# Kernel tuning notes

Hardware: AMD Instinct MI355X
Metric: run time of the kernel (lower is better)

The kernel has to match this reference:

```python
import jax, jax.numpy as jnp
import numpy as np

NUM_EMB = 8192
DIM = 64
DECAY = 0.99
EPS = 1e-05
COMMIT = 0.25


def setup_inputs() -> dict:
    key = jax.random.key(0)
    k1, k2, k3 = jax.random.split(key, 3)
    inputs = jax.random.normal(k1, (8, 4096, DIM), jnp.float32)
    weight = jax.random.normal(k2, (NUM_EMB, DIM), jnp.float32)
    ema_cluster_count = jnp.ones((NUM_EMB,), jnp.float32)
    ema_weight_sum = jax.random.normal(k3, (NUM_EMB, DIM), jnp.float32)
    return {
        'inputs': inputs,
        'weight': weight,
        'ema_cluster_count': ema_cluster_count,
        'ema_weight_sum': ema_weight_sum,
    }


def reference(inputs, weight, ema_cluster_count, ema_weight_sum):
    flat = inputs.reshape(-1, DIM)  # [N, D]
    distances = (
        jnp.sum(flat ** 2, axis=1, keepdims=True)
        + jnp.sum(weight ** 2, axis=1)
        - 2.0 * flat @ weight.T
    )
    idx = jnp.argmin(distances, axis=1)  # [N] int

    # EMA stats (training branch): one-hot column sums == segment counts,
    # encodings.T @ flat == segment sums of inputs by code index.
    counts = jax.ops.segment_sum(
        jnp.ones(flat.shape[0], jnp.float32), idx, num_segments=NUM_EMB)
    new_cc = ema_cluster_count * DECAY + (1.0 - DECAY) * counts
    emb_sum = jax.ops.segment_sum(flat, idx, num_segments=NUM_EMB)
    new_ws = ema_weight_sum * DECAY + (1.0 - DECAY) * emb_sum

    n = jnp.sum(new_cc)
    smoothed = (new_cc + EPS) / (n + NUM_EMB * EPS) * n
    new_weight = new_ws / smoothed[:, None]  # updated codebook [K, D]

    quantized_raw = new_weight[idx].reshape(inputs.shape)
    e_latent_loss = jnp.mean((jax.lax.stop_gradient(quantized_raw) - inputs) ** 2)
    vq_loss = COMMIT * e_latent_loss

    avg_probs = counts / flat.shape[0]
    perplexity = jnp.exp(-jnp.sum(avg_probs * jnp.log(avg_probs + 1e-10)))

    # straight-through estimator
    quantized = inputs + jax.lax.stop_gradient(quantized_raw - inputs)
    return quantized, vq_loss, idx, perplexity, new_weight, new_cc, new_ws
```

## Files before the change

### kernel.cpp

```cpp
#include <hip/hip_runtime.h>
#include <math.h>

typedef _Float16 f16x8 __attribute__((ext_vector_type(8)));
typedef float f32x4 __attribute__((ext_vector_type(4)));

#define NROWS 32768
#define KEMB  8192

#define DECAYF 0.99f
#define OMDF   0.01f

#define OUT_Q    0
#define OUT_LOSS 2097152
#define OUT_IDX  2097153
#define OUT_PERP 2129921
#define OUT_NW   2129922
#define OUT_NCC  2654210
#define OUT_NWS  2662402

#define WS_N      0
#define WS_ENT    1
#define WS_COUNTS 4
#define WS_EMB    8196
#define WS_IDX    532484
#define WS_W2H    565252
#define WS_WFRAG  573444
#define WS_ZERO_UNITS 532484

__device__ __forceinline__ float sq_rn(float v) { return __fmul_rn(v, v); }

__device__ __forceinline__ float npsumsq64(const float* vbuf) {
  float a[8];
#pragma unroll
  for (int j = 0; j < 8; ++j) a[j] = sq_rn(vbuf[j]);
#pragma unroll
  for (int m = 1; m < 8; ++m)
#pragma unroll
    for (int j = 0; j < 8; ++j) a[j] = __fadd_rn(a[j], sq_rn(vbuf[m*8 + j]));
  return __fadd_rn(__fadd_rn(__fadd_rn(a[0],a[1]), __fadd_rn(a[2],a[3])),
                   __fadd_rn(__fadd_rn(a[4],a[5]), __fadd_rn(a[6],a[7])));
}

__device__ __forceinline__ void split_f16(float x, _Float16& hi, _Float16& lo) {
  hi = (_Float16)x;
  float r = __fsub_rn(x, (float)hi);
  lo = (_Float16)r;
}

__global__ __launch_bounds__(256) void prep_kernel(const float* __restrict__ wg,
                                                   float* __restrict__ ws) {
  const int tid = blockIdx.x * 256 + threadIdx.x;
  if (tid < KEMB) {
    const float* src = wg + (size_t)tid * 64;
    float vbuf[64];
#pragma unroll
    for (int f = 0; f < 16; ++f) {
      float4 v = *(const float4*)(src + f*4);
      vbuf[f*4+0]=v.x; vbuf[f*4+1]=v.y; vbuf[f*4+2]=v.z; vbuf[f*4+3]=v.w;
    }
    ws[WS_W2H + tid] = __fmul_rn(0.5f, npsumsq64(vbuf));
  } else if (tid < KEMB + 65536) {
    const int u = tid - KEMB;
    const int K = u >> 3, g = u & 7;
    const int n = K & 15, P = K >> 4;
    const int slot = (g&3)*16 + n, shi = g >> 2;
    const float* src = wg + (size_t)K*64 + g*8;
    float4 v0 = *(const float4*)src, v1 = *(const float4*)(src + 4);
    float vv[8] = {v0.x,v0.y,v0.z,v0.w,v1.x,v1.y,v1.z,v1.w};
    f16x8 hi, lo;
#pragma unroll
    for (int j = 0; j < 8; ++j) { _Float16 h, l; split_f16(vv[j], h, l); hi[j]=h; lo[j]=l; }
    _Float16* wf = (_Float16*)(ws + WS_WFRAG);
    *(f16x8*)&wf[((size_t)(P*4 + shi)*64 + slot)*8]     = hi;
    *(f16x8*)&wf[((size_t)(P*4 + 2 + shi)*64 + slot)*8] = lo;
  }
}

#define COMPUTE_PANEL(I, B0, B1, B2, B3, W2)                                        \
  {                                                                                 \
    const f32x4 cin = {(W2), (W2), (W2), (W2)};                                     \
    f32x4 acc[4];                                                                   \
    _Pragma("unroll")                                                               \
    for (int rt = 0; rt < 4; ++rt) acc[rt] = __builtin_amdgcn_mfma_f32_16x16x32_f16(a[rt][0], (B0), cin, 0,0,0); \
    _Pragma("unroll")                                                               \
    for (int rt = 0; rt < 4; ++rt) acc[rt] = __builtin_amdgcn_mfma_f32_16x16x32_f16(a[rt][1], (B1), acc[rt], 0,0,0); \
    _Pragma("unroll")                                                               \
    for (int rt = 0; rt < 4; ++rt) acc[rt] = __builtin_amdgcn_mfma_f32_16x16x32_f16(a[rt][2], (B0), acc[rt], 0,0,0); \
    _Pragma("unroll")                                                               \
    for (int rt = 0; rt < 4; ++rt) acc[rt] = __builtin_amdgcn_mfma_f32_16x16x32_f16(a[rt][3], (B1), acc[rt], 0,0,0); \
    _Pragma("unroll")                                                               \
    for (int rt = 0; rt < 4; ++rt) acc[rt] = __builtin_amdgcn_mfma_f32_16x16x32_f16(a[rt][0], (B2), acc[rt], 0,0,0); \
    _Pragma("unroll")                                                               \
    for (int rt = 0; rt < 4; ++rt) acc[rt] = __builtin_amdgcn_mfma_f32_16x16x32_f16(a[rt][1], (B3), acc[rt], 0,0,0); \
    const int kk = (I)*64 + cg*16 + n16;                                            \
    _Pragma("unroll")                                                               \
    for (int rt = 0; rt < 4; ++rt)                                                  \
      _Pragma("unroll")                                                             \
      for (int reg = 0; reg < 4; ++reg) {                                           \
        const float dist = acc[rt][reg];                                            \
        const int bi = rt*4 + reg;                                                  \
        if (dist < best[bi]) { best[bi] = dist; bestk[bi] = kk; }                   \
      }                                                                             \
  }

#define LOADB(I, C0, C1, C2, C3, CW)                                                \
  {                                                                                 \
    const size_t base = ((size_t)((I)*4 + cg) * 256) * 8 + lane8;                   \
    C0 = *(const f16x8*)&wfrag[base];                                               \
    C1 = *(const f16x8*)&wfrag[base + 512];                                         \
    C2 = *(const f16x8*)&wfrag[base + 1024];                                        \
    C3 = *(const f16x8*)&wfrag[base + 1536];                                        \
    CW = w2hg[(I)*64 + cg*16 + n16];                                                \
  }

__global__ __launch_bounds__(512) void argmin_kernel(const float* __restrict__ xg,
                                                     float* __restrict__ out,
                                                     float* __restrict__ ws) {
  __shared__ __align__(16) _Float16 xp[8*4*64*8];
  __shared__ float md[128*4];
  __shared__ int   mk[128*4];
  __shared__ int   bkL[128];

  const int t    = threadIdx.x;
  const int lane = t & 63, wv = t >> 6;
  const int quad = lane >> 4, n16 = lane & 15;
  const int rg = wv >> 2, cg = wv & 3;
  const int row0 = blockIdx.x * 128;
  const _Float16* __restrict__ wfrag = (const _Float16*)(ws + WS_WFRAG);
  const float* __restrict__ w2hg = ws + WS_W2H;

#pragma unroll
  for (int it = 0; it < 2; ++it) {
    const int u  = t + 512*it;
    const int rp = u >> 7, n = (u >> 3) & 15, g = u & 7;
    const float* src = xg + (size_t)(row0 + rp*16 + n)*64 + g*8;
    float4 v0 = *(const float4*)src, v1 = *(const float4*)(src + 4);
    float vv[8] = {v0.x,v0.y,v0.z,v0.w,v1.x,v1.y,v1.z,v1.w};
    f16x8 hi, lo;
#pragma unroll
    for (int j = 0; j < 8; ++j) { _Float16 h, l; split_f16(-vv[j], h, l); hi[j]=h; lo[j]=l; }
    const int slot = (g&3)*16 + n, shi = g >> 2;
    *(f16x8*)&xp[(((rp*4) + shi)*64 + slot)*8]     = hi;
    *(f16x8*)&xp[(((rp*4) + 2 + shi)*64 + slot)*8] = lo;
  }
  __syncthreads();

  f16x8 a[4][4];
#pragma unroll
  for (int rt = 0; rt < 4; ++rt)
#pragma unroll
    for (int s = 0; s < 4; ++s)
      a[rt][s] = *(const f16x8*)&xp[(((rg*4+rt)*4 + s)*64 + lane)*8];

  float best[16]; int bestk[16];
#pragma unroll
  for (int i = 0; i < 16; ++i) { best[i] = INFINITY; bestk[i] = 0; }

  const size_t lane8 = (size_t)lane * 8;
  f16x8 p0, p1, p2, p3, q0, q1, q2, q3;
  float pw, qw;
  LOADB(0, p0, p1, p2, p3, pw);

  for (int it = 0; it < 128; it += 2) {
    LOADB(it+1, q0, q1, q2, q3, qw);
    COMPUTE_PANEL(it, p0, p1, p2, p3, pw);
    if (it + 2 < 128) LOADB(it+2, p0, p1, p2, p3, pw);
    COMPUTE_PANEL(it+1, q0, q1, q2, q3, qw);
  }

#pragma unroll
  for (int bi = 0; bi < 16; ++bi) {
    float bd = best[bi]; int bk = bestk[bi];
#pragma unroll
    for (int m = 1; m < 16; m <<= 1) {
      const float od = __shfl_xor(bd, m, 64);
      const int   ok = __shfl_xor(bk, m, 64);
      if (od < bd || (od == bd && ok < bk)) { bd = od; bk = ok; }
    }
    best[bi] = bd; bestk[bi] = bk;
  }
  if (n16 == 0) {
#pragma unroll
    for (int rt = 0; rt < 4; ++rt)
#pragma unroll
      for (int reg = 0; reg < 4; ++reg) {
        const int row = rg*64 + rt*16 + quad*4 + reg;
        md[row*4 + cg] = best[rt*4+reg];
        mk[row*4 + cg] = bestk[rt*4+reg];
      }
  }
  __syncthreads();

  if (t < 128) {
    const int row = t;
    float bd = md[row*4]; int bk = mk[row*4];
#pragma unroll
    for (int u = 1; u < 4; ++u) {
      const float d2 = md[row*4 + u]; const int k2 = mk[row*4 + u];
      if (d2 < bd || (d2 == bd && k2 < bk)) { bd = d2; bk = k2; }
    }
    out[OUT_IDX + row0 + row] = (float)bk;
    ((int*)ws)[WS_IDX + row0 + row] = bk;
    bkL[row] = bk;
    atomicAdd(&ws[WS_COUNTS + bk], 1.0f);
  }
  __syncthreads();

#pragma unroll 4
  for (int r = 0; r < 16; ++r) {
    const int row = wv*16 + r;
    const int k = bkL[row];
    atomicAdd(&ws[WS_EMB + (size_t)k*64 + lane],
              xg[(size_t)(row0 + row)*64 + lane]);
  }
}

__global__ __launch_bounds__(256) void stats_kernel(const float* __restrict__ cc,
                                                    float* __restrict__ out,
                                                    float* __restrict__ ws) {
  const int t = threadIdx.x;
  float v1 = 0.0f, v2 = 0.0f;
#pragma unroll
  for (int i = 0; i < 32; ++i) {
    const int k = i*256 + t;
    const float cnt = ws[WS_COUNTS + k];
    const float ncc = __fadd_rn(__fmul_rn(DECAYF, cc[k]), __fmul_rn(OMDF, cnt));
    out[OUT_NCC + k] = ncc;
    const float p = cnt * (1.0f/32768.0f);
    v1 += ncc;
    v2 += __fmul_rn(p, logf(__fadd_rn(p, 1e-10f)));
  }
#pragma unroll
  for (int off = 32; off > 0; off >>= 1) {
    v1 += __shfl_down(v1, off);
    v2 += __shfl_down(v2, off);
  }
  __shared__ float s1[4], s2[4];
  const int lane = t & 63, wid = t >> 6;
  if (lane == 0) { s1[wid] = v1; s2[wid] = v2; }
  __syncthreads();
  if (t == 0) {
    ws[WS_N]   = (s1[0]+s1[1]) + (s1[2]+s1[3]);
    ws[WS_ENT] = (s2[0]+s2[1]) + (s2[2]+s2[3]);
  }
}

__global__ __launch_bounds__(256) void update_kernel(const float* __restrict__ ws0,
                                                     float* __restrict__ out,
                                                     float* __restrict__ ws) {
  const int e4 = blockIdx.x * 256 + threadIdx.x;
  const int k = e4 >> 4;
  const float n = ws[WS_N];
  const float ncc = out[OUT_NCC + k];
  const float smoothed = __fmul_rn(__fadd_rn(ncc, 1e-5f) / __fadd_rn(n, 0.08192f), n);
  const float inv_s = 1.0f / smoothed;
  float4 w0 = *(const float4*)(ws0 + (size_t)e4*4);
  float4 em = *(const float4*)(ws + WS_EMB + (size_t)e4*4);
  float wv[4] = {w0.x, w0.y, w0.z, w0.w};
  float ev[4] = {em.x, em.y, em.z, em.w};
  float nwsv[4], nwv[4];
#pragma unroll
  for (int i = 0; i < 4; ++i) {
    nwsv[i] = __fadd_rn(__fmul_rn(DECAYF, wv[i]), __fmul_rn(OMDF, ev[i]));
    nwv[i]  = nwsv[i] / smoothed;
  }
  (void)inv_s;
  float4 onws = {nwsv[0], nwsv[1], nwsv[2], nwsv[3]};
  float4 onw  = {nwv[0],  nwv[1],  nwv[2],  nwv[3]};
  *(float4*)(out + OUT_NWS + (size_t)e4*4) = onws;
  *(float4*)(out + OUT_NW  + (size_t)e4*4) = onw;
  if (e4 == 0) out[OUT_PERP] = expf(-ws[WS_ENT]);
}

__global__ __launch_bounds__(256) void quant_kernel(const float* __restrict__ xg,
                                                    float* __restrict__ out,
                                                    float* __restrict__ ws) {
  const int t = threadIdx.x;
  const int* idxb = (const int*)ws + WS_IDX;
  float v = 0.0f;
#pragma unroll
  for (int j = 0; j < 4; ++j) {
    const int e4 = (j*512 + blockIdx.x)*256 + t;
    const int row = e4 >> 4, d = (e4 & 15) * 4;
    const int k = idxb[row];
    const float* nw = out + OUT_NW + (size_t)k*64 + d;
    float2 q0 = *(const float2*)nw, q1 = *(const float2*)(nw + 2);
    float4 x = *(const float4*)(xg + (size_t)e4*4);
    float qv[4] = {q0.x, q0.y, q1.x, q1.y};
    float xv[4] = {x.x, x.y, x.z, x.w};
    float4 o;
    float ov[4];
#pragma unroll
    for (int i = 0; i < 4; ++i) {
      const float df = __fsub_rn(qv[i], xv[i]);
      ov[i] = __fadd_rn(xv[i], df);
      v = fmaf(df, df, v);
    }
    o.x = ov[0]; o.y = ov[1]; o.z = ov[2]; o.w = ov[3];
    *(float4*)(out + OUT_Q + (size_t)e4*4) = o;
  }
#pragma unroll
  for (int off = 32; off > 0; off >>= 1) v += __shfl_down(v, off);
  __shared__ float sm[4];
  const int lane = t & 63, wid = t >> 6;
  if (lane == 0) sm[wid] = v;
  __syncthreads();
  if (t == 0) ws[WS_COUNTS + blockIdx.x] = (sm[0]+sm[1]) + (sm[2]+sm[3]);
}

__global__ void final_kernel(float* __restrict__ out, const float* __restrict__ ws) {
  const int t = threadIdx.x;
  float v = 0.0f;
#pragma unroll
  for (int i = 0; i < 8; ++i) v += ws[WS_COUNTS + i*64 + t];
#pragma unroll
  for (int off = 32; off > 0; off >>= 1) v += __shfl_down(v, off);
  if (t == 0) out[OUT_LOSS] = __fmul_rn(0.25f, v / 2097152.0f);
}

extern "C" void kernel_launch(void* const* d_in, const int* in_sizes, int n_in,
                              void* d_out, int out_size, void* d_ws, size_t ws_size,
                              hipStream_t stream) {
  (void)in_sizes; (void)n_in; (void)out_size; (void)ws_size;
  const float* x   = (const float*)d_in[0];
  const float* w   = (const float*)d_in[1];
  const float* cc  = (const float*)d_in[2];
  const float* ws0 = (const float*)d_in[3];
  float* out = (float*)d_out;
  float* ws  = (float*)d_ws;

  hipMemsetAsync(d_ws, 0, (size_t)WS_ZERO_UNITS * 4, stream);
  hipLaunchKernelGGL(prep_kernel,   dim3(288),  dim3(256), 0, stream, w, ws);
  hipLaunchKernelGGL(argmin_kernel, dim3(256),  dim3(512), 0, stream, x, out, ws);
  hipLaunchKernelGGL(stats_kernel,  dim3(1),    dim3(256), 0, stream, cc, out, ws);
  hipLaunchKernelGGL(update_kernel, dim3(512),  dim3(256), 0, stream, ws0, out, ws);
  hipLaunchKernelGGL(quant_kernel,  dim3(512),  dim3(256), 0, stream, x, out, ws);
  hipLaunchKernelGGL(final_kernel,  dim3(1),    dim3(64),  0, stream, out, ws);
}
```

Measured before the change: 187.8 us.

## Remove memset and stats kernel by folding zeroing, total-count algebra, and entropy into neighbors

Workspace zeroing moves from a separate memset into a grid-stride loop inside prep_kernel. The single-block stats kernel is removed. The total n is computed in prep as 0.99*sum(cc) plus 0.01*N, since the counts always sum to the row count. New cluster counts are computed inside update_kernel, and the entropy and perplexity reduction moves into final_kernel. This cuts two launches and a serial single-block step from the critical path. The loss partials now reuse the W2H workspace region, which is safe only because W2H is dead after argmin.

```diff
diff --git a/kernel.cpp b/kernel.cpp
--- a/kernel.cpp
+++ b/kernel.cpp
@@ -26,6 +26,7 @@
 #define WS_W2H    565252
 #define WS_WFRAG  573444
 #define WS_ZERO_UNITS 532484
+#define WS_LOSSP  (WS_W2H + 1024)
 
 __device__ __forceinline__ float sq_rn(float v) { return __fmul_rn(v, v); }
 
@@ -48,8 +49,10 @@
 }
 
 __global__ __launch_bounds__(256) void prep_kernel(const float* __restrict__ wg,
+                                                   const float* __restrict__ cc,
                                                    float* __restrict__ ws) {
   const int tid = blockIdx.x * 256 + threadIdx.x;
+  for (int i = tid; i < WS_ZERO_UNITS; i += 73728) ws[i] = 0.0f;
   if (tid < KEMB) {
     const float* src = wg + (size_t)tid * 64;
     float vbuf[64];
@@ -74,6 +77,18 @@
     *(f16x8*)&wf[((size_t)(P*4 + shi)*64 + slot)*8]     = hi;
     *(f16x8*)&wf[((size_t)(P*4 + 2 + shi)*64 + slot)*8] = lo;
   }
+  if (blockIdx.x == 0) {
+    float s = 0.0f;
+    for (int i = threadIdx.x; i < KEMB; i += 256) s += cc[i];
+#pragma unroll
+    for (int off = 32; off > 0; off >>= 1) s += __shfl_down(s, off);
+    __shared__ float sw[4];
+    const int lane = threadIdx.x & 63, wid = threadIdx.x >> 6;
+    if (lane == 0) sw[wid] = s;
+    __syncthreads();
+    if (threadIdx.x == 0)
+      ws[WS_N] = __fadd_rn(__fmul_rn(DECAYF, (sw[0]+sw[1])+(sw[2]+sw[3])), 327.68f);
+  }
 }
 
 #define COMPUTE_PANEL(I, B0, B1, B2, B3, W2)                                        \
@@ -215,45 +230,17 @@
   }
 }
 
-__global__ __launch_bounds__(256) void stats_kernel(const float* __restrict__ cc,
-                                                    float* __restrict__ out,
-                                                    float* __restrict__ ws) {
-  const int t = threadIdx.x;
-  float v1 = 0.0f, v2 = 0.0f;
-#pragma unroll
-  for (int i = 0; i < 32; ++i) {
-    const int k = i*256 + t;
-    const float cnt = ws[WS_COUNTS + k];
-    const float ncc = __fadd_rn(__fmul_rn(DECAYF, cc[k]), __fmul_rn(OMDF, cnt));
-    out[OUT_NCC + k] = ncc;
-    const float p = cnt * (1.0f/32768.0f);
-    v1 += ncc;
-    v2 += __fmul_rn(p, logf(__fadd_rn(p, 1e-10f)));
-  }
-#pragma unroll
-  for (int off = 32; off > 0; off >>= 1) {
-    v1 += __shfl_down(v1, off);
-    v2 += __shfl_down(v2, off);
-  }
-  __shared__ float s1[4], s2[4];
-  const int lane = t & 63, wid = t >> 6;
-  if (lane == 0) { s1[wid] = v1; s2[wid] = v2; }
-  __syncthreads();
-  if (t == 0) {
-    ws[WS_N]   = (s1[0]+s1[1]) + (s1[2]+s1[3]);
-    ws[WS_ENT] = (s2[0]+s2[1]) + (s2[2]+s2[3]);
-  }
-}
-
 __global__ __launch_bounds__(256) void update_kernel(const float* __restrict__ ws0,
+                                                     const float* __restrict__ cc,
                                                      float* __restrict__ out,
                                                      float* __restrict__ ws) {
   const int e4 = blockIdx.x * 256 + threadIdx.x;
   const int k = e4 >> 4;
   const float n = ws[WS_N];
-  const float ncc = out[OUT_NCC + k];
+  const float cnt = ws[WS_COUNTS + k];
+  const float ncc = __fadd_rn(__fmul_rn(DECAYF, cc[k]), __fmul_rn(OMDF, cnt));
+  if ((e4 & 15) == 0) out[OUT_NCC + k] = ncc;
   const float smoothed = __fmul_rn(__fadd_rn(ncc, 1e-5f) / __fadd_rn(n, 0.08192f), n);
-  const float inv_s = 1.0f / smoothed;
   float4 w0 = *(const float4*)(ws0 + (size_t)e4*4);
   float4 em = *(const float4*)(ws + WS_EMB + (size_t)e4*4);
   float wv[4] = {w0.x, w0.y, w0.z, w0.w};
@@ -264,12 +251,10 @@
     nwsv[i] = __fadd_rn(__fmul_rn(DECAYF, wv[i]), __fmul_rn(OMDF, ev[i]));
     nwv[i]  = nwsv[i] / smoothed;
   }
-  (void)inv_s;
   float4 onws = {nwsv[0], nwsv[1], nwsv[2], nwsv[3]};
   float4 onw  = {nwv[0],  nwv[1],  nwv[2],  nwv[3]};
   *(float4*)(out + OUT_NWS + (size_t)e4*4) = onws;
   *(float4*)(out + OUT_NW  + (size_t)e4*4) = onw;
-  if (e4 == 0) out[OUT_PERP] = expf(-ws[WS_ENT]);
 }
 
 __global__ __launch_bounds__(256) void quant_kernel(const float* __restrict__ xg,
@@ -305,17 +290,33 @@
   const int lane = t & 63, wid = t >> 6;
   if (lane == 0) sm[wid] = v;
   __syncthreads();
-  if (t == 0) ws[WS_COUNTS + blockIdx.x] = (sm[0]+sm[1]) + (sm[2]+sm[3]);
-}
-
-__global__ void final_kernel(float* __restrict__ out, const float* __restrict__ ws) {
+  if (t == 0) ws[WS_LOSSP + blockIdx.x] = (sm[0]+sm[1]) + (sm[2]+sm[3]);
+}
+
+__global__ __launch_bounds__(256) void final_kernel(float* __restrict__ out,
+                                                    const float* __restrict__ ws) {
   const int t = threadIdx.x;
-  float v = 0.0f;
-#pragma unroll
-  for (int i = 0; i < 8; ++i) v += ws[WS_COUNTS + i*64 + t];
-#pragma unroll
-  for (int off = 32; off > 0; off >>= 1) v += __shfl_down(v, off);
-  if (t == 0) out[OUT_LOSS] = __fmul_rn(0.25f, v / 2097152.0f);
+  float lv = ws[WS_LOSSP + t] + ws[WS_LOSSP + 256 + t];
+  float ev = 0.0f;
+#pragma unroll
+  for (int i = 0; i < 32; ++i) {
+    const float cnt = ws[WS_COUNTS + i*256 + t];
+    const float p = cnt * (1.0f/32768.0f);
+    ev += __fmul_rn(p, logf(__fadd_rn(p, 1e-10f)));
+  }
+#pragma unroll
+  for (int off = 32; off > 0; off >>= 1) {
+    lv += __shfl_down(lv, off);
+    ev += __shfl_down(ev, off);
+  }
+  __shared__ float s1[4], s2[4];
+  const int lane = t & 63, wid = t >> 6;
+  if (lane == 0) { s1[wid] = lv; s2[wid] = ev; }
+  __syncthreads();
+  if (t == 0) {
+    out[OUT_LOSS] = __fmul_rn(0.25f, ((s1[0]+s1[1])+(s1[2]+s1[3])) / 2097152.0f);
+    out[OUT_PERP] = expf(-((s2[0]+s2[1])+(s2[2]+s2[3])));
+  }
 }
 
 extern "C" void kernel_launch(void* const* d_in, const int* in_sizes, int n_in,
@@ -329,11 +330,9 @@
   float* out = (float*)d_out;
   float* ws  = (float*)d_ws;
 
-  hipMemsetAsync(d_ws, 0, (size_t)WS_ZERO_UNITS * 4, stream);
-  hipLaunchKernelGGL(prep_kernel,   dim3(288),  dim3(256), 0, stream, w, ws);
-  hipLaunchKernelGGL(argmin_kernel, dim3(256),  dim3(512), 0, stream, x, out, ws);
-  hipLaunchKernelGGL(stats_kernel,  dim3(1),    dim3(256), 0, stream, cc, out, ws);
-  hipLaunchKernelGGL(update_kernel, dim3(512),  dim3(256), 0, stream, ws0, out, ws);
-  hipLaunchKernelGGL(quant_kernel,  dim3(512),  dim3(256), 0, stream, x, out, ws);
-  hipLaunchKernelGGL(final_kernel,  dim3(1),    dim3(64),  0, stream, out, ws);
-}
+  hipLaunchKernelGGL(prep_kernel,   dim3(288), dim3(256), 0, stream, w, cc, ws);
+  hipLaunchKernelGGL(argmin_kernel, dim3(256), dim3(512), 0, stream, x, out, ws);
+  hipLaunchKernelGGL(update_kernel, dim3(512), dim3(256), 0, stream, ws0, cc, out, ws);
+  hipLaunchKernelGGL(quant_kernel,  dim3(512), dim3(256), 0, stream, x, out, ws);
+  hipLaunchKernelGGL(final_kernel,  dim3(1),   dim3(256), 0, stream, out, ws);
+}
```

New measurement: 189.9 us. Within noise of the previous version (+1.1%).
